# Optimization experiments

Measured on AMD Instinct MI355X. Metric: run time of the kernel, lower is better.

## Reference

```python
import jax, jax.numpy as jnp
import numpy as np

EMBED = 1024
B, S = 8, 2048

def setup_inputs() -> dict:
    key = jax.random.key(0)
    k1, k2 = jax.random.split(key)
    x = jax.random.normal(k1, (B, S, EMBED), dtype=jnp.float32)
    # torch Linear(embed, 3*embed): store weight already transposed as [E, 3E]
    W_qkv = jax.random.normal(k2, (EMBED, 3 * EMBED), dtype=jnp.float32) * (1.0 / np.sqrt(EMBED))
    b_qkv = jnp.zeros((3 * EMBED,), dtype=jnp.float32)
    return {"x": x, "W_qkv": W_qkv, "b_qkv": b_qkv}

def reference(x, W_qkv, b_qkv):
    E = x.shape[-1]
    qkv = x @ W_qkv + b_qkv                      # [B,S,3E]
    Q, K, V = jnp.split(qkv, 3, axis=-1)         # each [B,S,E]
    scale = 1.0 / jnp.sqrt(jnp.asarray(E, x.dtype))
    scores = jnp.einsum('bqe,bke->bqk', Q, K) * scale  # [B,S,S]
    attn = jax.nn.softmax(scores, axis=-1)
    return jnp.einsum('bqk,bke->bqe', attn, V)   # [B,S,E]
```

## Files before the change

### kernel.cpp

```cpp
#include <hip/hip_runtime.h>

typedef unsigned short u16;
typedef unsigned int u32;
typedef __attribute__((ext_vector_type(8))) short short8;
typedef __attribute__((ext_vector_type(4))) short short4v;
typedef __attribute__((ext_vector_type(4))) float f32x4;

__device__ __forceinline__ u16 f2bf(float f) {
    u32 u = __float_as_uint(f);
    u32 r = (u + 0x7fffu + ((u >> 16) & 1u)) >> 16;
    return (u16)r;
}
__device__ __forceinline__ float bf2f(u16 h) {
    return __uint_as_float(((u32)h) << 16);
}

__device__ __forceinline__ void gload_lds16(const void* g, void* l) {
    __builtin_amdgcn_global_load_lds((const __attribute__((address_space(1))) void*)g,
                                     (__attribute__((address_space(3))) void*)l, 16, 0, 0);
}

#define BARRIER() do { __builtin_amdgcn_sched_barrier(0); __builtin_amdgcn_s_barrier(); __builtin_amdgcn_sched_barrier(0); } while (0)
#define VMCNT(N)  asm volatile("s_waitcnt vmcnt(" #N ")" ::: "memory")

#define STAGE(ptr, LDG, LOFF, RBASE, kelem) \
    do { gload_lds16((ptr) + (size_t)(RBASE) * (LDG) + (kelem),        lds + (LOFF) + ((RBASE) + (wid << 3)) * 128); \
         gload_lds16((ptr) + (size_t)((RBASE) + 64) * (LDG) + (kelem), lds + (LOFF) + ((RBASE) + 64 + (wid << 3)) * 128); } while (0)

template<int ROFF, int QH>
__device__ __forceinline__ void ld_a(short8 (&a)[4][2], const char* lds, int arow, int c0, int c1) {
    #pragma unroll
    for (int mf = 0; mf < 4; ++mf) {
        a[mf][0] = *(const short8*)(lds + ROFF + QH * 16384 + mf * 2048 + arow + c0);
        a[mf][1] = *(const short8*)(lds + ROFF + QH * 16384 + mf * 2048 + arow + c1);
    }
}
template<int ROFF, int QH>
__device__ __forceinline__ void ld_b(short8 (&b)[2][2], const char* lds, int brow, int c0, int c1) {
    #pragma unroll
    for (int nf = 0; nf < 2; ++nf) {
        b[nf][0] = *(const short8*)(lds + ROFF + QH * 16384 + nf * 2048 + brow + c0);
        b[nf][1] = *(const short8*)(lds + ROFF + QH * 16384 + nf * 2048 + brow + c1);
    }
}

template<int QM, int QN>
__device__ __forceinline__ void mfq(f32x4 (&acc)[2][4][2][2], short8 (&a)[4][2], short8 (&b)[2][2]) {
    __builtin_amdgcn_s_setprio(1);
    #pragma unroll
    for (int mf = 0; mf < 4; ++mf)
        #pragma unroll
        for (int nf = 0; nf < 2; ++nf) {
            acc[QM][mf][QN][nf] = __builtin_amdgcn_mfma_f32_16x16x32_bf16(a[mf][0], b[nf][0], acc[QM][mf][QN][nf], 0, 0, 0);
            acc[QM][mf][QN][nf] = __builtin_amdgcn_mfma_f32_16x16x32_bf16(a[mf][1], b[nf][1], acc[QM][mf][QN][nf], 0, 0, 0);
        }
    __builtin_amdgcn_s_setprio(0);
}

template<int EPI, int LDA, int LDB, int LDC, int K>
__global__ __launch_bounds__(512, 2)
void gemm8p(const u16* __restrict__ A, long long sA,
            const u16* __restrict__ B, long long sB,
            void* __restrict__ Cv, long long sC,
            const float* __restrict__ bias, float scale,
            int GX, int GY)
{
    extern __shared__ char lds[];
    const int tid  = threadIdx.x;
    const int wid  = tid >> 6;
    const int lane = tid & 63;

    const int nwg = gridDim.x;
    int bid = blockIdx.x;
    bid = (bid & 7) * (nwg >> 3) + (bid >> 3);
    const int bx  = bid % GX;
    const int rem = bid / GX;
    const int by  = rem % GY;
    const long long z = rem / GY;

    const int bm = by * 256, bn = bx * 256;
    const u16* Atile = A + z * sA + (size_t)bm * LDA;
    const u16* Btile = B + z * sB + (size_t)bn * LDB;

    const int wm = wid >> 2, wn = wid & 3;
    const int l15   = lane & 15;
    const int lxor  = (lane & 7) << 4;
    const int khi   = (lane >> 4) << 4;
    const int colk0 = khi ^ lxor;
    const int colk1 = (64 + khi) ^ lxor;
    const int arow  = (wm * 64 + l15) * 128;
    const int brow  = (wn * 32 + l15) * 128;

    const int swz = ((lane & 7) ^ (lane >> 3)) << 3;
    const u16* pA = Atile + (size_t)((wid << 3) + (lane >> 3)) * LDA + swz;
    const u16* pB = Btile + (size_t)((wid << 3) + (lane >> 3)) * LDB + swz;

    f32x4 acc[2][4][2][2];
    #pragma unroll
    for (int i = 0; i < 2; ++i)
        #pragma unroll
        for (int m = 0; m < 4; ++m)
            #pragma unroll
            for (int j = 0; j < 2; ++j)
                #pragma unroll
                for (int n = 0; n < 2; ++n)
                    acc[i][m][j][n] = (f32x4){0.f, 0.f, 0.f, 0.f};

    STAGE(pA, LDA, 0,     0,   0);  STAGE(pB, LDB, 32768, 0,   0);
    STAGE(pA, LDA, 0,     128, 0);  STAGE(pB, LDB, 32768, 128, 0);
    STAGE(pB, LDB, 98304, 0,   64); STAGE(pA, LDA, 65536, 0,   64);
    STAGE(pB, LDB, 98304, 128, 64); STAGE(pA, LDA, 65536, 128, 64);
    VMCNT(8);
    BARRIER();

    short8 a[4][2], b0[2][2], b1[2][2];
    const int NI = K >> 7;

    for (int it = 0; it < NI; ++it) {
        const bool more = (it + 1 < NI);
        const int kn = it * 128 + 128;
        ld_a<0, 0>(a, lds, arow, colk0, colk1);
        ld_b<32768, 0>(b0, lds, brow, colk0, colk1);
        BARRIER(); mfq<0, 0>(acc, a, b0); BARRIER();
        ld_b<32768, 1>(b1, lds, brow, colk0, colk1);
        if (more) STAGE(pB, LDB, 32768, 0, kn);
        BARRIER(); mfq<0, 1>(acc, a, b1); BARRIER();
        ld_a<0, 1>(a, lds, arow, colk0, colk1);
        if (more) STAGE(pA, LDA, 0, 0, kn);
        BARRIER(); mfq<1, 1>(acc, a, b1); BARRIER();
        if (more) { STAGE(pB, LDB, 32768, 128, kn); STAGE(pA, LDA, 0, 128, kn); VMCNT(8); }
        else      { VMCNT(0); }
        BARRIER(); mfq<1, 0>(acc, a, b0); BARRIER();
        ld_a<65536, 0>(a, lds, arow, colk0, colk1);
        ld_b<98304, 0>(b0, lds, brow, colk0, colk1);
        BARRIER(); mfq<0, 0>(acc, a, b0); BARRIER();
        ld_b<98304, 1>(b1, lds, brow, colk0, colk1);
        if (more) STAGE(pB, LDB, 98304, 0, kn + 64);
        BARRIER(); mfq<0, 1>(acc, a, b1); BARRIER();
        ld_a<65536, 1>(a, lds, arow, colk0, colk1);
        if (more) STAGE(pA, LDA, 65536, 0, kn + 64);
        BARRIER(); mfq<1, 1>(acc, a, b1); BARRIER();
        if (more) { STAGE(pB, LDB, 98304, 128, kn + 64); STAGE(pA, LDA, 65536, 128, kn + 64); VMCNT(8); }
        BARRIER(); mfq<1, 0>(acc, a, b0); BARRIER();
    }

    const int r0 = (lane >> 4) * 4;
    const int cc = lane & 15;
    #pragma unroll
    for (int qn = 0; qn < 2; ++qn)
        #pragma unroll
        for (int nf = 0; nf < 2; ++nf) {
            const int col = bn + qn * 128 + wn * 32 + nf * 16 + cc;
            const float badd = (EPI == 0) ? bias[col] : 0.f;
            #pragma unroll
            for (int qm = 0; qm < 2; ++qm)
                #pragma unroll
                for (int mf = 0; mf < 4; ++mf) {
                    const int row = bm + qm * 128 + wm * 64 + mf * 16 + r0;
                    #pragma unroll
                    for (int r = 0; r < 4; ++r) {
                        const float v = acc[qm][mf][qn][nf][r] * scale + badd;
                        if (EPI == 2) ((float*)Cv + z * sC)[(size_t)(row + r) * LDC + col] = v;
                        else          ((u16*)Cv + z * sC)[(size_t)(row + r) * LDC + col] = f2bf(v);
                    }
                }
        }
}

__global__ __launch_bounds__(256)
void cvt_f32_bf16(const float* __restrict__ in, u16* __restrict__ out, int n8)
{
    const int i = blockIdx.x * 256 + threadIdx.x;
    if (i >= n8) return;
    const float4* p = (const float4*)in;
    const float4 a = p[2 * i], b = p[2 * i + 1];
    short8 o;
    o[0] = (short)f2bf(a.x); o[1] = (short)f2bf(a.y);
    o[2] = (short)f2bf(a.z); o[3] = (short)f2bf(a.w);
    o[4] = (short)f2bf(b.x); o[5] = (short)f2bf(b.y);
    o[6] = (short)f2bf(b.z); o[7] = (short)f2bf(b.w);
    ((short8*)out)[i] = o;
}

__global__ __launch_bounds__(256)
void cvt_w_t(const float* __restrict__ W, u16* __restrict__ Wt)
{
    __shared__ u16 T[32][33];
    const int tid = threadIdx.x;
    const int tr = tid >> 3;
    const int tc = (tid & 7) * 4;
    const int c0 = blockIdx.x * 32;
    const int r0 = blockIdx.y * 32;
    const float4 v = *(const float4*)&W[(size_t)(r0 + tr) * 3072 + c0 + tc];
    T[tr][tc + 0] = f2bf(v.x); T[tr][tc + 1] = f2bf(v.y);
    T[tr][tc + 2] = f2bf(v.z); T[tr][tc + 3] = f2bf(v.w);
    __syncthreads();
    short4v o;
    o[0] = (short)T[tc + 0][tr]; o[1] = (short)T[tc + 1][tr];
    o[2] = (short)T[tc + 2][tr]; o[3] = (short)T[tc + 3][tr];
    *(short4v*)&Wt[(size_t)(c0 + tr) * 1024 + r0 + tc] = o;
}

__global__ __launch_bounds__(256)
void trans_v(const u16* __restrict__ qkv, u16* __restrict__ Vt)
{
    __shared__ u16 T[32][33];
    const int tid = threadIdx.x;
    const int tr = tid >> 3;
    const int tc = (tid & 7) * 4;
    const int e0 = blockIdx.x * 32;
    const int s0 = blockIdx.y * 32;
    const int b  = blockIdx.z;
    const short4v v = *(const short4v*)&qkv[(size_t)(b * 2048 + s0 + tr) * 3072 + 2048 + e0 + tc];
    T[tr][tc + 0] = (u16)v[0]; T[tr][tc + 1] = (u16)v[1];
    T[tr][tc + 2] = (u16)v[2]; T[tr][tc + 3] = (u16)v[3];
    __syncthreads();
    short4v o;
    o[0] = (short)T[tc + 0][tr]; o[1] = (short)T[tc + 1][tr];
    o[2] = (short)T[tc + 2][tr]; o[3] = (short)T[tc + 3][tr];
    *(short4v*)&Vt[(size_t)b * 1024 * 2048 + (size_t)(e0 + tr) * 2048 + s0 + tc] = o;
}

__global__ __launch_bounds__(256)
void softmax_bf16(u16* __restrict__ S)
{
    u16* row = S + (size_t)blockIdx.x * 2048;
    const int tid  = threadIdx.x;
    const int wid  = tid >> 6;
    const int lane = tid & 63;
    __shared__ float red[4];

    const short8 v8 = *(const short8*)&row[tid * 8];
    float v[8];
    float m = -3.4e38f;
    #pragma unroll
    for (int j = 0; j < 8; ++j) { v[j] = bf2f((u16)v8[j]); m = fmaxf(m, v[j]); }
    #pragma unroll
    for (int off = 32; off; off >>= 1) m = fmaxf(m, __shfl_xor(m, off));
    if (lane == 0) red[wid] = m;
    __syncthreads();
    m = fmaxf(fmaxf(red[0], red[1]), fmaxf(red[2], red[3]));
    float s = 0.f;
    #pragma unroll
    for (int j = 0; j < 8; ++j) { v[j] = __expf(v[j] - m); s += v[j]; }
    #pragma unroll
    for (int off = 32; off; off >>= 1) s += __shfl_xor(s, off);
    __syncthreads();
    if (lane == 0) red[wid] = s;
    __syncthreads();
    s = red[0] + red[1] + red[2] + red[3];
    const float inv = 1.f / s;
    short8 o;
    #pragma unroll
    for (int j = 0; j < 8; ++j) o[j] = (short)f2bf(v[j] * inv);
    *(short8*)&row[tid * 8] = o;
}

extern "C" void kernel_launch(void* const* d_in, const int* in_sizes, int n_in,
                              void* d_out, int out_size, void* d_ws, size_t ws_size,
                              hipStream_t stream) {
    const float* x    = (const float*)d_in[0];
    const float* W    = (const float*)d_in[1];
    const float* bias = (const float*)d_in[2];
    float* out = (float*)d_out;

    const int B = 8, S = 2048, E = 1024, N3 = 3072;
    const int M = B * S;

    char* ws = (char*)d_ws;
    u16* xb   = (u16*)ws;
    u16* Wtb  = (u16*)(ws + 33554432);
    u16* qkvb = (u16*)(ws + 39845888);
    u16* Vtb  = (u16*)(ws + 140509184);
    u16* Sb   = (u16*)(ws + 174063616);

    const size_t need_full = 174063616ull + (size_t)B * S * S * 2;
    const bool full = ws_size >= need_full;
    const float sc = 1.0f / 32.0f;
    const int LDSB = 131072;

    auto kQKV = gemm8p<0, 1024, 1024, 3072, 1024>;
    auto kQKT = gemm8p<1, 3072, 3072, 2048, 1024>;
    auto kPV  = gemm8p<2, 2048, 2048, 1024, 2048>;
    (void)hipFuncSetAttribute(reinterpret_cast<const void*>(kQKV),
                              hipFuncAttributeMaxDynamicSharedMemorySize, LDSB);
    (void)hipFuncSetAttribute(reinterpret_cast<const void*>(kQKT),
                              hipFuncAttributeMaxDynamicSharedMemorySize, LDSB);
    (void)hipFuncSetAttribute(reinterpret_cast<const void*>(kPV),
                              hipFuncAttributeMaxDynamicSharedMemorySize, LDSB);

    cvt_f32_bf16<<<dim3((M * E) / 8 / 256), 256, 0, stream>>>(x, xb, (M * E) / 8);
    cvt_w_t<<<dim3(96, 32), 256, 0, stream>>>(W, Wtb);

    kQKV<<<dim3(12 * 64), 512, LDSB, stream>>>(xb, 0, Wtb, 0, qkvb, 0, bias, 1.0f, 12, 64);

    trans_v<<<dim3(32, 64, 8), 256, 0, stream>>>(qkvb, Vtb);

    if (full) {
        kQKT<<<dim3(8 * 8 * 8), 512, LDSB, stream>>>(
            qkvb, (long long)S * N3, qkvb + E, (long long)S * N3,
            Sb, (long long)S * S, nullptr, sc, 8, 8);
        softmax_bf16<<<dim3(B * S), 256, 0, stream>>>(Sb);
        kPV<<<dim3(4 * 8 * 8), 512, LDSB, stream>>>(
            Sb, (long long)S * S, Vtb, (long long)E * S,
            out, (long long)S * E, nullptr, 1.0f, 4, 8);
    } else {
        for (int b = 0; b < B; ++b) {
            const u16* Qb = qkvb + (size_t)b * S * N3;
            kQKT<<<dim3(8 * 8), 512, LDSB, stream>>>(
                Qb, 0, Qb + E, 0, Sb, 0, nullptr, sc, 8, 8);
            softmax_bf16<<<dim3(S), 256, 0, stream>>>(Sb);
            kPV<<<dim3(4 * 8), 512, LDSB, stream>>>(
                Sb, 0, Vtb + (size_t)b * E * S, 0,
                out + (size_t)b * S * E, 0, nullptr, 1.0f, 4, 8);
        }
    }
}
```

Measured before the change: 292.7 us.

## Reschedule GEMM LDS prefetch stages and halve barriers per MFMA phase

Reorders the global-to-LDS STAGE loads in the 8-phase GEMM main loop so prefetches of the next K slice are issued at different points, adjusts the vmcnt waits to match, and removes the trailing barrier after each MFMA block. The aim is fewer workgroup synchronisations and better overlap of memory loads with matrix cores. The risk is LDS races: one A sub-tile of the second half-buffer is now staged inside the same iteration in which it is consumed, so correctness depends on the waits and barrier placement being exactly right.

Result: faster. 280.5 us (-4.1%).

```diff
diff --git a/kernel.cpp b/kernel.cpp
--- a/kernel.cpp
+++ b/kernel.cpp
@@ -108,9 +108,9 @@
 
     STAGE(pA, LDA, 0,     0,   0);  STAGE(pB, LDB, 32768, 0,   0);
     STAGE(pA, LDA, 0,     128, 0);  STAGE(pB, LDB, 32768, 128, 0);
-    STAGE(pB, LDB, 98304, 0,   64); STAGE(pA, LDA, 65536, 0,   64);
-    STAGE(pB, LDB, 98304, 128, 64); STAGE(pA, LDA, 65536, 128, 64);
-    VMCNT(8);
+    STAGE(pA, LDA, 65536, 0,   64);
+    STAGE(pB, LDB, 98304, 0,   64); STAGE(pB, LDB, 98304, 128, 64);
+    VMCNT(6);
     BARRIER();
 
     short8 a[4][2], b0[2][2], b1[2][2];
@@ -118,30 +118,31 @@
 
     for (int it = 0; it < NI; ++it) {
         const bool more = (it + 1 < NI);
-        const int kn = it * 128 + 128;
+        const int kc0 = it * 128;
+        const int kn  = kc0 + 128;
         ld_a<0, 0>(a, lds, arow, colk0, colk1);
         ld_b<32768, 0>(b0, lds, brow, colk0, colk1);
-        BARRIER(); mfq<0, 0>(acc, a, b0); BARRIER();
+        STAGE(pA, LDA, 65536, 128, kc0 + 64);
+        BARRIER(); mfq<0, 0>(acc, a, b0);
         ld_b<32768, 1>(b1, lds, brow, colk0, colk1);
-        if (more) STAGE(pB, LDB, 32768, 0, kn);
-        BARRIER(); mfq<0, 1>(acc, a, b1); BARRIER();
+        BARRIER(); mfq<0, 1>(acc, a, b1);
         ld_a<0, 1>(a, lds, arow, colk0, colk1);
-        if (more) STAGE(pA, LDA, 0, 0, kn);
-        BARRIER(); mfq<1, 1>(acc, a, b1); BARRIER();
-        if (more) { STAGE(pB, LDB, 32768, 128, kn); STAGE(pA, LDA, 0, 128, kn); VMCNT(8); }
+        BARRIER(); mfq<1, 1>(acc, a, b1);
+        if (more) { STAGE(pA, LDA, 0, 0, kn); STAGE(pB, LDB, 32768, 0, kn); VMCNT(4); }
         else      { VMCNT(0); }
-        BARRIER(); mfq<1, 0>(acc, a, b0); BARRIER();
+        BARRIER(); mfq<1, 0>(acc, a, b0);
         ld_a<65536, 0>(a, lds, arow, colk0, colk1);
         ld_b<98304, 0>(b0, lds, brow, colk0, colk1);
-        BARRIER(); mfq<0, 0>(acc, a, b0); BARRIER();
+        if (more) { STAGE(pA, LDA, 0, 128, kn); STAGE(pB, LDB, 32768, 128, kn); }
+        BARRIER(); mfq<0, 0>(acc, a, b0);
         ld_b<98304, 1>(b1, lds, brow, colk0, colk1);
-        if (more) STAGE(pB, LDB, 98304, 0, kn + 64);
-        BARRIER(); mfq<0, 1>(acc, a, b1); BARRIER();
+        BARRIER(); mfq<0, 1>(acc, a, b1);
         ld_a<65536, 1>(a, lds, arow, colk0, colk1);
-        if (more) STAGE(pA, LDA, 65536, 0, kn + 64);
-        BARRIER(); mfq<1, 1>(acc, a, b1); BARRIER();
-        if (more) { STAGE(pB, LDB, 98304, 128, kn + 64); STAGE(pA, LDA, 65536, 128, kn + 64); VMCNT(8); }
-        BARRIER(); mfq<1, 0>(acc, a, b0); BARRIER();
+        BARRIER(); mfq<1, 1>(acc, a, b1);
+        if (more) { STAGE(pA, LDA, 65536, 0, kn + 64);
+                    STAGE(pB, LDB, 98304, 0, kn + 64); STAGE(pB, LDB, 98304, 128, kn + 64);
+                    VMCNT(6); }
+        BARRIER(); mfq<1, 0>(acc, a, b0);
     }
 
     const int r0 = (lane >> 4) * 4;
```

## Replace 256x256 8-wave GEMM with 128x128 4-wave double-buffered kernel

Applied to the files above, without the earlier changes.

Rewrites the bf16 GEMM used for the QKV projection, QK^T and PV. It moves from 256x256 tiles with 8 waves and a 128KB LDS quad-buffer to 128x128 tiles with 4 waves and a 64KB double-buffered pipeline. The loop issues fewer barriers, prefetches one k-half ahead with vmcnt waits, and quadruples the grid. This trades lower data reuse per tile and more global traffic for more workgroups per CU and simpler synchronisation.

Result: slower. 311.5 us (+6.5%).

```diff
diff --git a/kernel.cpp b/kernel.cpp
--- a/kernel.cpp
+++ b/kernel.cpp
@@ -23,43 +23,49 @@
 #define BARRIER() do { __builtin_amdgcn_sched_barrier(0); __builtin_amdgcn_s_barrier(); __builtin_amdgcn_sched_barrier(0); } while (0)
 #define VMCNT(N)  asm volatile("s_waitcnt vmcnt(" #N ")" ::: "memory")
 
-#define STAGE(ptr, LDG, LOFF, RBASE, kelem) \
-    do { gload_lds16((ptr) + (size_t)(RBASE) * (LDG) + (kelem),        lds + (LOFF) + ((RBASE) + (wid << 3)) * 128); \
-         gload_lds16((ptr) + (size_t)((RBASE) + 64) * (LDG) + (kelem), lds + (LOFF) + ((RBASE) + 64 + (wid << 3)) * 128); } while (0)
-
-template<int ROFF, int QH>
-__device__ __forceinline__ void ld_a(short8 (&a)[4][2], const char* lds, int arow, int c0, int c1) {
+#define STG1(ptr, LDG, LOFF, RBASE, kelem) \
+    gload_lds16((ptr) + (size_t)(RBASE) * (LDG) + (kelem), lds + (LOFF) + ((RBASE) + (wid << 3)) * 128)
+
+#define STG_A(LOFF, kelem) do { \
+    STG1(pA, LDA, LOFF, 0,  kelem); STG1(pA, LDA, LOFF, 32, kelem); \
+    STG1(pA, LDA, LOFF, 64, kelem); STG1(pA, LDA, LOFF, 96, kelem); } while (0)
+#define STG_B(LOFF, kelem) do { \
+    STG1(pB, LDB, LOFF, 0,  kelem); STG1(pB, LDB, LOFF, 64, kelem); \
+    STG1(pB, LDB, LOFF, 32, kelem); STG1(pB, LDB, LOFF, 96, kelem); } while (0)
+
+template<int BOFF>
+__device__ __forceinline__ void ld_a4(short8 (&a)[4][2], const char* lds, int arow, int c0, int c1) {
     #pragma unroll
     for (int mf = 0; mf < 4; ++mf) {
-        a[mf][0] = *(const short8*)(lds + ROFF + QH * 16384 + mf * 2048 + arow + c0);
-        a[mf][1] = *(const short8*)(lds + ROFF + QH * 16384 + mf * 2048 + arow + c1);
-    }
-}
-template<int ROFF, int QH>
-__device__ __forceinline__ void ld_b(short8 (&b)[2][2], const char* lds, int brow, int c0, int c1) {
+        a[mf][0] = *(const short8*)(lds + BOFF + mf * 2048 + arow + c0);
+        a[mf][1] = *(const short8*)(lds + BOFF + mf * 2048 + arow + c1);
+    }
+}
+template<int BOFF, int P>
+__device__ __forceinline__ void ld_b2(short8 (&b)[2][2], const char* lds, int brow, int c0, int c1) {
     #pragma unroll
     for (int nf = 0; nf < 2; ++nf) {
-        b[nf][0] = *(const short8*)(lds + ROFF + QH * 16384 + nf * 2048 + brow + c0);
-        b[nf][1] = *(const short8*)(lds + ROFF + QH * 16384 + nf * 2048 + brow + c1);
-    }
-}
-
-template<int QM, int QN>
-__device__ __forceinline__ void mfq(f32x4 (&acc)[2][4][2][2], short8 (&a)[4][2], short8 (&b)[2][2]) {
+        b[nf][0] = *(const short8*)(lds + BOFF + P * 4096 + nf * 2048 + brow + c0);
+        b[nf][1] = *(const short8*)(lds + BOFF + P * 4096 + nf * 2048 + brow + c1);
+    }
+}
+
+template<int P>
+__device__ __forceinline__ void mfq2(f32x4 (&acc)[4][4], short8 (&a)[4][2], short8 (&b)[2][2]) {
     __builtin_amdgcn_s_setprio(1);
     #pragma unroll
     for (int mf = 0; mf < 4; ++mf)
         #pragma unroll
         for (int nf = 0; nf < 2; ++nf) {
-            acc[QM][mf][QN][nf] = __builtin_amdgcn_mfma_f32_16x16x32_bf16(a[mf][0], b[nf][0], acc[QM][mf][QN][nf], 0, 0, 0);
-            acc[QM][mf][QN][nf] = __builtin_amdgcn_mfma_f32_16x16x32_bf16(a[mf][1], b[nf][1], acc[QM][mf][QN][nf], 0, 0, 0);
+            acc[mf][P * 2 + nf] = __builtin_amdgcn_mfma_f32_16x16x32_bf16(a[mf][0], b[nf][0], acc[mf][P * 2 + nf], 0, 0, 0);
+            acc[mf][P * 2 + nf] = __builtin_amdgcn_mfma_f32_16x16x32_bf16(a[mf][1], b[nf][1], acc[mf][P * 2 + nf], 0, 0, 0);
         }
     __builtin_amdgcn_s_setprio(0);
 }
 
 template<int EPI, int LDA, int LDB, int LDC, int K>
-__global__ __launch_bounds__(512, 2)
-void gemm8p(const u16* __restrict__ A, long long sA,
+__global__ __launch_bounds__(256, 2)
+void gemm2p(const u16* __restrict__ A, long long sA,
             const u16* __restrict__ B, long long sB,
             void* __restrict__ Cv, long long sC,
             const float* __restrict__ bias, float scale,
@@ -78,93 +84,82 @@
     const int by  = rem % GY;
     const long long z = rem / GY;
 
-    const int bm = by * 256, bn = bx * 256;
+    const int bm = by * 128, bn = bx * 128;
     const u16* Atile = A + z * sA + (size_t)bm * LDA;
     const u16* Btile = B + z * sB + (size_t)bn * LDB;
 
-    const int wm = wid >> 2, wn = wid & 3;
+    const int wm = wid >> 1, wn = wid & 1;
     const int l15   = lane & 15;
     const int lxor  = (lane & 7) << 4;
     const int khi   = (lane >> 4) << 4;
     const int colk0 = khi ^ lxor;
     const int colk1 = (64 + khi) ^ lxor;
     const int arow  = (wm * 64 + l15) * 128;
-    const int brow  = (wn * 32 + l15) * 128;
-
-    const int swz = ((lane & 7) ^ (lane >> 3)) << 3;
+    const int brow  = (wn * 64 + l15) * 128;
+
+    const int swz = ((lane & 7) ^ ((lane >> 3) & 7)) << 3;
     const u16* pA = Atile + (size_t)((wid << 3) + (lane >> 3)) * LDA + swz;
     const u16* pB = Btile + (size_t)((wid << 3) + (lane >> 3)) * LDB + swz;
 
-    f32x4 acc[2][4][2][2];
-    #pragma unroll
-    for (int i = 0; i < 2; ++i)
+    f32x4 acc[4][4];
+    #pragma unroll
+    for (int m = 0; m < 4; ++m)
         #pragma unroll
-        for (int m = 0; m < 4; ++m)
-            #pragma unroll
-            for (int j = 0; j < 2; ++j)
-                #pragma unroll
-                for (int n = 0; n < 2; ++n)
-                    acc[i][m][j][n] = (f32x4){0.f, 0.f, 0.f, 0.f};
-
-    STAGE(pA, LDA, 0,     0,   0);  STAGE(pB, LDB, 32768, 0,   0);
-    STAGE(pA, LDA, 0,     128, 0);  STAGE(pB, LDB, 32768, 128, 0);
-    STAGE(pB, LDB, 98304, 0,   64); STAGE(pA, LDA, 65536, 0,   64);
-    STAGE(pB, LDB, 98304, 128, 64); STAGE(pA, LDA, 65536, 128, 64);
-    VMCNT(8);
-    BARRIER();
-
-    short8 a[4][2], b0[2][2], b1[2][2];
+        for (int n = 0; n < 4; ++n)
+            acc[m][n] = (f32x4){0.f, 0.f, 0.f, 0.f};
+
+    STG_A(0, 0);
+    STG_B(16384, 0);
+
+    short8 a[4][2], b[2][2];
     const int NI = K >> 7;
 
     for (int it = 0; it < NI; ++it) {
         const bool more = (it + 1 < NI);
-        const int kn = it * 128 + 128;
-        ld_a<0, 0>(a, lds, arow, colk0, colk1);
-        ld_b<32768, 0>(b0, lds, brow, colk0, colk1);
-        BARRIER(); mfq<0, 0>(acc, a, b0); BARRIER();
-        ld_b<32768, 1>(b1, lds, brow, colk0, colk1);
-        if (more) STAGE(pB, LDB, 32768, 0, kn);
-        BARRIER(); mfq<0, 1>(acc, a, b1); BARRIER();
-        ld_a<0, 1>(a, lds, arow, colk0, colk1);
-        if (more) STAGE(pA, LDA, 0, 0, kn);
-        BARRIER(); mfq<1, 1>(acc, a, b1); BARRIER();
-        if (more) { STAGE(pB, LDB, 32768, 128, kn); STAGE(pA, LDA, 0, 128, kn); VMCNT(8); }
-        else      { VMCNT(0); }
-        BARRIER(); mfq<1, 0>(acc, a, b0); BARRIER();
-        ld_a<65536, 0>(a, lds, arow, colk0, colk1);
-        ld_b<98304, 0>(b0, lds, brow, colk0, colk1);
-        BARRIER(); mfq<0, 0>(acc, a, b0); BARRIER();
-        ld_b<98304, 1>(b1, lds, brow, colk0, colk1);
-        if (more) STAGE(pB, LDB, 98304, 0, kn + 64);
-        BARRIER(); mfq<0, 1>(acc, a, b1); BARRIER();
-        ld_a<65536, 1>(a, lds, arow, colk0, colk1);
-        if (more) STAGE(pA, LDA, 65536, 0, kn + 64);
-        BARRIER(); mfq<1, 1>(acc, a, b1); BARRIER();
-        if (more) { STAGE(pB, LDB, 98304, 128, kn + 64); STAGE(pA, LDA, 65536, 128, kn + 64); VMCNT(8); }
-        BARRIER(); mfq<1, 0>(acc, a, b0); BARRIER();
+        const int ka = (it << 7) + 64;
+        const int kb = (it << 7) + 128;
+
+        VMCNT(2); BARRIER();
+        ld_a4<0>(a, lds, arow, colk0, colk1);
+        ld_b2<16384, 0>(b, lds, brow, colk0, colk1);
+        STG_A(32768, ka);
+        mfq2<0>(acc, a, b);
+
+        VMCNT(4); BARRIER();
+        ld_b2<16384, 1>(b, lds, brow, colk0, colk1);
+        STG_B(49152, ka);
+        mfq2<1>(acc, a, b);
+
+        VMCNT(2); BARRIER();
+        ld_a4<32768>(a, lds, arow, colk0, colk1);
+        ld_b2<49152, 0>(b, lds, brow, colk0, colk1);
+        if (more) STG_A(0, kb);
+        mfq2<0>(acc, a, b);
+
+        if (more) { VMCNT(4); } else { VMCNT(0); }
+        BARRIER();
+        ld_b2<49152, 1>(b, lds, brow, colk0, colk1);
+        if (more) STG_B(16384, kb);
+        mfq2<1>(acc, a, b);
     }
 
     const int r0 = (lane >> 4) * 4;
     const int cc = lane & 15;
     #pragma unroll
-    for (int qn = 0; qn < 2; ++qn)
+    for (int nf = 0; nf < 4; ++nf) {
+        const int col = bn + wn * 64 + nf * 16 + cc;
+        const float badd = (EPI == 0) ? bias[col] : 0.f;
         #pragma unroll
-        for (int nf = 0; nf < 2; ++nf) {
-            const int col = bn + qn * 128 + wn * 32 + nf * 16 + cc;
-            const float badd = (EPI == 0) ? bias[col] : 0.f;
+        for (int mf = 0; mf < 4; ++mf) {
+            const int row = bm + wm * 64 + mf * 16 + r0;
             #pragma unroll
-            for (int qm = 0; qm < 2; ++qm)
-                #pragma unroll
-                for (int mf = 0; mf < 4; ++mf) {
-                    const int row = bm + qm * 128 + wm * 64 + mf * 16 + r0;
-                    #pragma unroll
-                    for (int r = 0; r < 4; ++r) {
-                        const float v = acc[qm][mf][qn][nf][r] * scale + badd;
-                        if (EPI == 2) ((float*)Cv + z * sC)[(size_t)(row + r) * LDC + col] = v;
-                        else          ((u16*)Cv + z * sC)[(size_t)(row + r) * LDC + col] = f2bf(v);
-                    }
-                }
+            for (int r = 0; r < 4; ++r) {
+                const float v = acc[mf][nf][r] * scale + badd;
+                if (EPI == 2) ((float*)Cv + z * sC)[(size_t)(row + r) * LDC + col] = v;
+                else          ((u16*)Cv + z * sC)[(size_t)(row + r) * LDC + col] = f2bf(v);
+            }
         }
+    }
 }
 
 __global__ __launch_bounds__(256)
@@ -277,11 +272,11 @@
     const size_t need_full = 174063616ull + (size_t)B * S * S * 2;
     const bool full = ws_size >= need_full;
     const float sc = 1.0f / 32.0f;
-    const int LDSB = 131072;
-
-    auto kQKV = gemm8p<0, 1024, 1024, 3072, 1024>;
-    auto kQKT = gemm8p<1, 3072, 3072, 2048, 1024>;
-    auto kPV  = gemm8p<2, 2048, 2048, 1024, 2048>;
+    const int LDSB = 65536;
+
+    auto kQKV = gemm2p<0, 1024, 1024, 3072, 1024>;
+    auto kQKT = gemm2p<1, 3072, 3072, 2048, 1024>;
+    auto kPV  = gemm2p<2, 2048, 2048, 1024, 2048>;
     (void)hipFuncSetAttribute(reinterpret_cast<const void*>(kQKV),
                               hipFuncAttributeMaxDynamicSharedMemorySize, LDSB);
     (void)hipFuncSetAttribute(reinterpret_cast<const void*>(kQKT),
@@ -292,27 +287,27 @@
     cvt_f32_bf16<<<dim3((M * E) / 8 / 256), 256, 0, stream>>>(x, xb, (M * E) / 8);
     cvt_w_t<<<dim3(96, 32), 256, 0, stream>>>(W, Wtb);
 
-    kQKV<<<dim3(12 * 64), 512, LDSB, stream>>>(xb, 0, Wtb, 0, qkvb, 0, bias, 1.0f, 12, 64);
+    kQKV<<<dim3(24 * 128), 256, LDSB, stream>>>(xb, 0, Wtb, 0, qkvb, 0, bias, 1.0f, 24, 128);
 
     trans_v<<<dim3(32, 64, 8), 256, 0, stream>>>(qkvb, Vtb);
 
     if (full) {
-        kQKT<<<dim3(8 * 8 * 8), 512, LDSB, stream>>>(
+        kQKT<<<dim3(16 * 16 * 8), 256, LDSB, stream>>>(
             qkvb, (long long)S * N3, qkvb + E, (long long)S * N3,
-            Sb, (long long)S * S, nullptr, sc, 8, 8);
+            Sb, (long long)S * S, nullptr, sc, 16, 16);
         softmax_bf16<<<dim3(B * S), 256, 0, stream>>>(Sb);
-        kPV<<<dim3(4 * 8 * 8), 512, LDSB, stream>>>(
+        kPV<<<dim3(8 * 16 * 8), 256, LDSB, stream>>>(
             Sb, (long long)S * S, Vtb, (long long)E * S,
-            out, (long long)S * E, nullptr, 1.0f, 4, 8);
+            out, (long long)S * E, nullptr, 1.0f, 8, 16);
     } else {
         for (int b = 0; b < B; ++b) {
             const u16* Qb = qkvb + (size_t)b * S * N3;
-            kQKT<<<dim3(8 * 8), 512, LDSB, stream>>>(
-                Qb, 0, Qb + E, 0, Sb, 0, nullptr, sc, 8, 8);
+            kQKT<<<dim3(16 * 16), 256, LDSB, stream>>>(
+                Qb, 0, Qb + E, 0, Sb, 0, nullptr, sc, 16, 16);
             softmax_bf16<<<dim3(S), 256, 0, stream>>>(Sb);
-            kPV<<<dim3(4 * 8), 512, LDSB, stream>>>(
+            kPV<<<dim3(8 * 16), 256, LDSB, stream>>>(
                 Sb, 0, Vtb + (size_t)b * E * S, 0,
-                out + (size_t)b * S * E, 0, nullptr, 1.0f, 4, 8);
+                out + (size_t)b * S * E, 0, nullptr, 1.0f, 8, 16);
         }
     }
 }
```
